# Kernel optimization log

Hardware: AMD Instinct MI355X
Metric: run time of the kernel (lower is better)

Reference implementation:

```python
import jax, jax.numpy as jnp
import numpy as np

LOAD_BALANCE_WEIGHT = 0.05


def setup_inputs() -> dict:
    key = jax.random.key(0)
    ks = jax.random.split(key, 8)
    B, H, C, E = 8192, 4096, 1000, 4
    s_h = 1.0 / np.sqrt(H)
    return {
        "x": jax.random.normal(ks[0], (B, H), dtype=jnp.float32),
        "Wr": jax.random.normal(ks[1], (H, E), dtype=jnp.float32) * s_h,
        "br": jnp.zeros((E,), dtype=jnp.float32),
        "W1": jax.random.normal(ks[2], (E, H, H), dtype=jnp.float32) * s_h,
        "b1": jnp.zeros((E, H), dtype=jnp.float32),
        "W2": jax.random.normal(ks[3], (E, H, C), dtype=jnp.float32) * s_h,
        "b2": jnp.zeros((E, C), dtype=jnp.float32),
    }


def reference(x, Wr, br, W1, b1, W2, b2):
    # Router: linear gate -> softmax probs (eval mode: no noise)
    E = Wr.shape[1]
    router_logits = x @ Wr + br                     # [B, E]
    routing_weights = jax.nn.softmax(router_logits, axis=-1)
    # Hard top-1 dispatch
    idx = jnp.argmax(routing_weights, axis=-1)      # [B]
    onehot = jax.nn.one_hot(idx, E, dtype=x.dtype)  # [B, E]
    # Switch-style load-balance loss: E * sum(fraction_e * mean_prob_e)
    frac = onehot.mean(axis=0)                      # [E]
    mean_p = routing_weights.mean(axis=0)           # [E]
    load_balance_loss = LOAD_BALANCE_WEIGHT * E * jnp.sum(frac * mean_p)
    # Dense all-expert compute, then hard-select per token (same math as
    # gather/scatter dispatch in the torch loop, fully vectorized)
    h = jax.nn.gelu(jnp.einsum('bh,ehk->ebk', x, W1) + b1[:, None, :])  # [E,B,H]
    expert_out = jnp.einsum('ebk,ekc->ebc', h, W2) + b2[:, None, :]     # [E,B,C]
    logits = jnp.einsum('be,ebc->bc', onehot, expert_out)               # [B,C]
    return logits, load_balance_loss, routing_weights
```

## Files before the change

### kernel.cpp

```cpp
#include <hip/hip_runtime.h>
#include <hip/hip_bf16.h>

#define NB 8192
#define NH 4096
#define NC 1000
#define NE 4
#define NCP 1024

typedef __attribute__((ext_vector_type(4))) float f32x4;
typedef __attribute__((ext_vector_type(8))) short s16x8;
typedef __attribute__((ext_vector_type(4))) unsigned int u32x4;

__device__ __forceinline__ unsigned cvtpk(float a, float b){
  unsigned r; asm("v_cvt_pk_bf16_f32 %0, %1, %2" : "=v"(r) : "v"(a), "v"(b)); return r;
}
__device__ __forceinline__ int swz_off(int r, int s){
  return (r << 6) + (((s ^ (r ^ (r >> 2))) & 3) << 4);
}
__device__ __forceinline__ int fswz(int r){ return (r ^ (r >> 2)) & 3; }

__device__ __forceinline__ void gload16(const void* g, void* l) {
  __builtin_amdgcn_global_load_lds(
      (const __attribute__((address_space(1))) unsigned int*)g,
      (__attribute__((address_space(3))) unsigned int*)l, 16, 0, 0);
}

__global__ __launch_bounds__(256) void router2_k(
    const float* __restrict__ x, const float* __restrict__ Wr,
    const float* __restrict__ br, float* __restrict__ out,
    int* __restrict__ idx, int* __restrict__ cnt_part, float* __restrict__ sum_part,
    __hip_bfloat16* __restrict__ xb)
{
  int b = blockIdx.x, t = threadIdx.x;
  const float* xr = x + (size_t)b * NH;
  int h0 = t << 4;
  f32x4 v[4];
  #pragma unroll
  for (int j = 0; j < 4; j++) v[j] = *(const f32x4*)(xr + h0 + (j << 2));
  u32x4 ob0 = { cvtpk(v[0][0],v[0][1]), cvtpk(v[0][2],v[0][3]),
                cvtpk(v[1][0],v[1][1]), cvtpk(v[1][2],v[1][3]) };
  u32x4 ob1 = { cvtpk(v[2][0],v[2][1]), cvtpk(v[2][2],v[2][3]),
                cvtpk(v[3][0],v[3][1]), cvtpk(v[3][2],v[3][3]) };
  *(u32x4*)(xb + (size_t)b * NH + h0) = ob0;
  *(u32x4*)(xb + (size_t)b * NH + h0 + 8) = ob1;

  double a0=0, a1=0, a2=0, a3=0;
  #pragma unroll
  for (int i = 0; i < 16; i++) {
    float xv = v[i >> 2][i & 3];
    f32x4 w = *(const f32x4*)(Wr + (size_t)(h0 + i) * 4);
    double xd = (double)xv;
    a0 += xd * (double)w[0]; a1 += xd * (double)w[1];
    a2 += xd * (double)w[2]; a3 += xd * (double)w[3];
  }
  for (int off = 32; off; off >>= 1) {
    a0 += __shfl_down(a0, off); a1 += __shfl_down(a1, off);
    a2 += __shfl_down(a2, off); a3 += __shfl_down(a3, off);
  }
  __shared__ double red[4][4];
  int wid = t >> 6;
  if ((t & 63) == 0) { red[wid][0]=a0; red[wid][1]=a1; red[wid][2]=a2; red[wid][3]=a3; }
  __syncthreads();
  if (t == 0) {
    double l[4];
    for (int e = 0; e < 4; e++)
      l[e] = red[0][e] + red[1][e] + red[2][e] + red[3][e] + (double)br[e];
    int am = 0; double mx = l[0];
    for (int e = 1; e < 4; e++) if (l[e] > mx) { mx = l[e]; am = e; }
    double p[4], s = 0;
    for (int e = 0; e < 4; e++) { p[e] = exp(l[e] - mx); s += p[e]; }
    float* rw = out + (size_t)NB * NC + 1 + (size_t)b * 4;
    int bin = (b & 63) * 4;
    for (int e = 0; e < 4; e++) {
      float pe = (float)(p[e] / s);
      rw[e] = pe;
      atomicAdd(&sum_part[bin + e], pe);
    }
    idx[b] = am;
    atomicAdd(&cnt_part[bin + am], 1);
  }
}

__global__ __launch_bounds__(256) void router_k(
    const float* __restrict__ x, const float* __restrict__ Wr,
    const float* __restrict__ br, float* __restrict__ out,
    int* __restrict__ idx, int* __restrict__ cnt_part, float* __restrict__ sum_part)
{
  int b = blockIdx.x, t = threadIdx.x;
  const float* xr = x + (size_t)b * NH;
  double a0=0, a1=0, a2=0, a3=0;
  for (int i = 0; i < 16; i++) {
    int h = t + (i << 8);
    float xv = xr[h];
    f32x4 w = *(const f32x4*)(Wr + (size_t)h * 4);
    double xd = (double)xv;
    a0 += xd * (double)w[0]; a1 += xd * (double)w[1];
    a2 += xd * (double)w[2]; a3 += xd * (double)w[3];
  }
  for (int off = 32; off; off >>= 1) {
    a0 += __shfl_down(a0, off); a1 += __shfl_down(a1, off);
    a2 += __shfl_down(a2, off); a3 += __shfl_down(a3, off);
  }
  __shared__ double red[4][4];
  int wid = t >> 6;
  if ((t & 63) == 0) { red[wid][0]=a0; red[wid][1]=a1; red[wid][2]=a2; red[wid][3]=a3; }
  __syncthreads();
  if (t == 0) {
    double l[4];
    for (int e = 0; e < 4; e++)
      l[e] = red[0][e] + red[1][e] + red[2][e] + red[3][e] + (double)br[e];
    int am = 0; double mx = l[0];
    for (int e = 1; e < 4; e++) if (l[e] > mx) { mx = l[e]; am = e; }
    double p[4], s = 0;
    for (int e = 0; e < 4; e++) { p[e] = exp(l[e] - mx); s += p[e]; }
    float* rw = out + (size_t)NB * NC + 1 + (size_t)b * 4;
    int bin = (b & 63) * 4;
    for (int e = 0; e < 4; e++) {
      float pe = (float)(p[e] / s);
      rw[e] = pe;
      atomicAdd(&sum_part[bin + e], pe);
    }
    idx[b] = am;
    atomicAdd(&cnt_part[bin + am], 1);
  }
}

__global__ void finalize_k(const int* __restrict__ cnt_part, const float* __restrict__ sum_part,
                           int* __restrict__ counts, int* __restrict__ offs, float* __restrict__ out)
{
  int t = threadIdx.x;
  __shared__ int cc[4]; __shared__ float ss[4];
  if (t < 4) {
    int c = 0; float s = 0;
    for (int i = 0; i < 64; i++) { c += cnt_part[i*4 + t]; s += sum_part[i*4 + t]; }
    cc[t] = c; ss[t] = s; counts[t] = c;
  }
  __syncthreads();
  if (t == 0) {
    int o = 0; float loss = 0.f;
    for (int e = 0; e < 4; e++) {
      offs[e] = o; o += cc[e];
      loss += ((float)cc[e] / (float)NB) * (ss[e] / (float)NB);
    }
    out[(size_t)NB * NC] = 0.05f * (float)NE * loss;
  }
}

__global__ __launch_bounds__(256) void scatter_k(
    const int* __restrict__ idx, const int* __restrict__ offs,
    int* __restrict__ cursors, int* __restrict__ perm)
{
  int b = blockIdx.x * 256 + threadIdx.x;
  int e = idx[b];
  int lane = threadIdx.x & 63;
  for (int e2 = 0; e2 < 4; e2++) {
    unsigned long long m = __ballot(e == e2);
    if (e == e2) {
      int nbelow = __popcll(m & ((1ULL << lane) - 1ULL));
      int base = 0;
      if (nbelow == 0) base = atomicAdd(&cursors[e2], (int)__popcll(m));
      int src = __ffsll((long long)m) - 1;
      base = __shfl(base, src);
      perm[offs[e2] + base + nbelow] = b;
    }
  }
}

__global__ __launch_bounds__(256) void transpose_k(
    const float* __restrict__ in, __hip_bfloat16* __restrict__ outp,
    int R, int C, int Cout)
{
  int e = blockIdx.z;
  int r0 = blockIdx.y << 5;
  int c0 = blockIdx.x << 10;
  const float* ine = in + (size_t)e * R * C;
  __hip_bfloat16* oute = outp + (size_t)e * Cout * R;
  int t = threadIdx.x;
  int c = c0 + (t << 2);
  unsigned o[4][16];
  if (c < C) {
    #pragma unroll
    for (int rp = 0; rp < 16; rp++) {
      f32x4 v0 = *(const f32x4*)(ine + (size_t)(r0 + 2*rp)     * C + c);
      f32x4 v1 = *(const f32x4*)(ine + (size_t)(r0 + 2*rp + 1) * C + c);
      #pragma unroll
      for (int j = 0; j < 4; j++) o[j][rp] = cvtpk(v0[j], v1[j]);
    }
  } else {
    #pragma unroll
    for (int j = 0; j < 4; j++)
      #pragma unroll
      for (int rp = 0; rp < 16; rp++) o[j][rp] = 0;
  }
  #pragma unroll
  for (int j = 0; j < 4; j++) {
    u32x4* dst = (u32x4*)(oute + (size_t)(c + j) * R + r0);
    dst[0] = (u32x4){ o[j][0],  o[j][1],  o[j][2],  o[j][3]  };
    dst[1] = (u32x4){ o[j][4],  o[j][5],  o[j][6],  o[j][7]  };
    dst[2] = (u32x4){ o[j][8],  o[j][9],  o[j][10], o[j][11] };
    dst[3] = (u32x4){ o[j][12], o[j][13], o[j][14], o[j][15] };
  }
}

__global__ __launch_bounds__(256) void gemm1n_k(
    const __hip_bfloat16* __restrict__ xb, const __hip_bfloat16* __restrict__ W1t,
    const float* __restrict__ b1, const int* __restrict__ perm,
    const int* __restrict__ counts, const int* __restrict__ offs,
    __hip_bfloat16* __restrict__ H1)
{
  int e = blockIdx.z;
  int cnt = counts[e];
  int m0 = blockIdx.y << 7;
  if (m0 >= cnt) return;
  int seg = offs[e];
  int n0 = blockIdx.x << 7;
  const __hip_bfloat16* W1te = W1t + (size_t)e * NH * NH;

  __shared__ __align__(16) char As[8192];
  __shared__ __align__(16) char Bs[8192];
  __shared__ int rowtok[128];

  int t = threadIdx.x;
  if (t < 128) {
    int rr = m0 + t; if (rr >= cnt) rr = cnt - 1;
    rowtok[t] = perm[seg + rr];
  }
  __syncthreads();

  int r0 = t >> 2, s0 = t & 3;
  int r1 = r0 + 64;
  const __hip_bfloat16* pA0 = xb + (size_t)rowtok[r0] * NH + ((s0 ^ fswz(r0)) << 3);
  const __hip_bfloat16* pA1 = xb + (size_t)rowtok[r1] * NH + ((s0 ^ fswz(r1)) << 3);
  const __hip_bfloat16* pB0 = W1te + (size_t)(n0 + r0) * NH + ((s0 ^ fswz(r0)) << 3);
  const __hip_bfloat16* pB1 = W1te + (size_t)(n0 + r1) * NH + ((s0 ^ fswz(r1)) << 3);
  int wid = t >> 6;
  char* ldsA0 = As + (wid << 10);
  char* ldsA1 = As + 4096 + (wid << 10);
  char* ldsB0 = Bs + (wid << 10);
  char* ldsB1 = Bs + 4096 + (wid << 10);

  f32x4 acc[4][4] = {};

  int lane = t & 63;
  int wm = (wid >> 1) << 6, wn = (wid & 1) << 6;
  int g = lane >> 4, cx = lane & 15;
  int aoff[4], boff[4];
  #pragma unroll
  for (int f = 0; f < 4; f++) {
    aoff[f] = swz_off(wm + (f << 4) + cx, g);
    boff[f] = swz_off(wn + (f << 4) + cx, g);
  }

  for (int kt = 0; kt < NH; kt += 32) {
    gload16(pA0 + kt, ldsA0);
    gload16(pA1 + kt, ldsA1);
    gload16(pB0 + kt, ldsB0);
    gload16(pB1 + kt, ldsB1);
    __syncthreads();
    s16x8 af[4], bfr[4];
    #pragma unroll
    for (int f = 0; f < 4; f++) {
      af[f]  = *(const s16x8*)(As + aoff[f]);
      bfr[f] = *(const s16x8*)(Bs + boff[f]);
    }
    #pragma unroll
    for (int mf = 0; mf < 4; mf++)
      #pragma unroll
      for (int nf = 0; nf < 4; nf++)
        acc[mf][nf] = __builtin_amdgcn_mfma_f32_16x16x32_bf16(af[mf], bfr[nf], acc[mf][nf], 0, 0, 0);
    __syncthreads();
  }

  const float* b1e = b1 + (size_t)e * NH;
  #pragma unroll
  for (int nf = 0; nf < 4; nf++) {
    int n = n0 + wn + (nf << 4) + cx;
    float bias = b1e[n];
    #pragma unroll
    for (int mf = 0; mf < 4; mf++) {
      #pragma unroll
      for (int i = 0; i < 4; i++) {
        int mseg = m0 + wm + (mf << 4) + (g << 2) + i;
        if (mseg < cnt) {
          float u = acc[mf][nf][i] + bias;
          float th = tanhf(0.79788456080286535588f * (u + 0.044715f * u * u * u));
          float hv = 0.5f * u * (1.0f + th);
          H1[(size_t)(seg + mseg) * NH + n] = __float2bfloat16(hv);
        }
      }
    }
  }
}

__global__ __launch_bounds__(256) void gemm2n_k(
    const __hip_bfloat16* __restrict__ H1, const __hip_bfloat16* __restrict__ W2t,
    const float* __restrict__ b2, const int* __restrict__ perm,
    const int* __restrict__ counts, const int* __restrict__ offs,
    float* __restrict__ out)
{
  int e = blockIdx.z;
  int cnt = counts[e];
  int m0 = blockIdx.y << 7;
  if (m0 >= cnt) return;
  int seg = offs[e];
  int n0 = blockIdx.x << 7;
  const __hip_bfloat16* W2te = W2t + (size_t)e * NCP * NH;

  __shared__ __align__(16) char As[8192];
  __shared__ __align__(16) char Bs[8192];
  __shared__ int rowtok[128];

  int t = threadIdx.x;
  if (t < 128) {
    int rr = m0 + t; if (rr >= cnt) rr = cnt - 1;
    rowtok[t] = perm[seg + rr];
  }
  __syncthreads();

  int r0 = t >> 2, s0 = t & 3;
  int r1 = r0 + 64;
  int rA0 = m0 + r0; if (rA0 >= cnt) rA0 = cnt - 1;
  int rA1 = m0 + r1; if (rA1 >= cnt) rA1 = cnt - 1;
  const __hip_bfloat16* pA0 = H1 + (size_t)(seg + rA0) * NH + ((s0 ^ fswz(r0)) << 3);
  const __hip_bfloat16* pA1 = H1 + (size_t)(seg + rA1) * NH + ((s0 ^ fswz(r1)) << 3);
  const __hip_bfloat16* pB0 = W2te + (size_t)(n0 + r0) * NH + ((s0 ^ fswz(r0)) << 3);
  const __hip_bfloat16* pB1 = W2te + (size_t)(n0 + r1) * NH + ((s0 ^ fswz(r1)) << 3);
  int wid = t >> 6;
  char* ldsA0 = As + (wid << 10);
  char* ldsA1 = As + 4096 + (wid << 10);
  char* ldsB0 = Bs + (wid << 10);
  char* ldsB1 = Bs + 4096 + (wid << 10);

  f32x4 acc[4][4] = {};

  int lane = t & 63;
  int wm = (wid >> 1) << 6, wn = (wid & 1) << 6;
  int g = lane >> 4, cx = lane & 15;
  int aoff[4], boff[4];
  #pragma unroll
  for (int f = 0; f < 4; f++) {
    aoff[f] = swz_off(wm + (f << 4) + cx, g);
    boff[f] = swz_off(wn + (f << 4) + cx, g);
  }

  for (int kt = 0; kt < NH; kt += 32) {
    gload16(pA0 + kt, ldsA0);
    gload16(pA1 + kt, ldsA1);
    gload16(pB0 + kt, ldsB0);
    gload16(pB1 + kt, ldsB1);
    __syncthreads();
    s16x8 af[4], bfr[4];
    #pragma unroll
    for (int f = 0; f < 4; f++) {
      af[f]  = *(const s16x8*)(As + aoff[f]);
      bfr[f] = *(const s16x8*)(Bs + boff[f]);
    }
    #pragma unroll
    for (int mf = 0; mf < 4; mf++)
      #pragma unroll
      for (int nf = 0; nf < 4; nf++)
        acc[mf][nf] = __builtin_amdgcn_mfma_f32_16x16x32_bf16(af[mf], bfr[nf], acc[mf][nf], 0, 0, 0);
    __syncthreads();
  }

  const float* b2e = b2 + (size_t)e * NC;
  #pragma unroll
  for (int nf = 0; nf < 4; nf++) {
    int n = n0 + wn + (nf << 4) + cx;
    if (n < NC) {
      float bias = b2e[n];
      #pragma unroll
      for (int mf = 0; mf < 4; mf++) {
        #pragma unroll
        for (int i = 0; i < 4; i++) {
          int mseg = m0 + wm + (mf << 4) + (g << 2) + i;
          if (mseg < cnt) {
            int tok = rowtok[wm + (mf << 4) + (g << 2) + i];
            out[(size_t)tok * NC + n] = acc[mf][nf][i] + bias;
          }
        }
      }
    }
  }
}

__global__ __launch_bounds__(256) void gemm1_k(
    const float* __restrict__ x, const float* __restrict__ W1,
    const float* __restrict__ b1, const int* __restrict__ perm,
    const int* __restrict__ counts, const int* __restrict__ offs,
    __hip_bfloat16* __restrict__ H1)
{
  int e = blockIdx.z;
  int cnt = counts[e];
  int m0 = blockIdx.y << 7;
  if (m0 >= cnt) return;
  int seg = offs[e];
  int n0 = blockIdx.x << 7;
  const float* W1e = W1 + (size_t)e * NH * NH;

  __shared__ __align__(16) char As[128*32*2];
  __shared__ __align__(16) char Bs[128*32*2];
  __shared__ int rowtok[128];

  int t = threadIdx.x;
  if (t < 128) {
    int rr = m0 + t; if (rr >= cnt) rr = cnt - 1;
    rowtok[t] = perm[seg + rr];
  }
  __syncthreads();

  int ar0 = t >> 2, as_ = t & 3;
  int ar1 = ar0 + 64;
  const float* asrc0 = x + (size_t)rowtok[ar0] * NH + (as_ << 3);
  const float* asrc1 = x + (size_t)rowtok[ar1] * NH + (as_ << 3);
  int aw0 = swz_off(ar0, as_), aw1 = swz_off(ar1, as_);
  int bnc = t & 31, bkp = t >> 5;
  const float* bsrc0 = W1e + (size_t)(bkp << 1) * NH + n0 + (bnc << 2);
  const float* bsrc1 = bsrc0 + (size_t)16 * NH;

  f32x4 acc[4][4] = {};

  int lane = t & 63, wid = t >> 6;
  int wm = (wid >> 1) << 6, wn = (wid & 1) << 6;
  int g = lane >> 4, cx = lane & 15;
  int aoff[4], boff[4];
  #pragma unroll
  for (int f = 0; f < 4; f++) {
    aoff[f] = swz_off(wm + (f << 4) + cx, g);
    boff[f] = swz_off(wn + (f << 4) + cx, g);
  }

  for (int kt = 0; kt < NH; kt += 32) {
    {
      f32x4 v0 = *(const f32x4*)(asrc0 + kt);
      f32x4 v1 = *(const f32x4*)(asrc0 + kt + 4);
      u32x4 w = { cvtpk(v0[0],v0[1]), cvtpk(v0[2],v0[3]), cvtpk(v1[0],v1[1]), cvtpk(v1[2],v1[3]) };
      *(u32x4*)(As + aw0) = w;
      f32x4 u0 = *(const f32x4*)(asrc1 + kt);
      f32x4 u1 = *(const f32x4*)(asrc1 + kt + 4);
      u32x4 w2 = { cvtpk(u0[0],u0[1]), cvtpk(u0[2],u0[3]), cvtpk(u1[0],u1[1]), cvtpk(u1[2],u1[3]) };
      *(u32x4*)(As + aw1) = w2;
    }
    {
      const float* p0 = bsrc0 + (size_t)kt * NH;
      f32x4 rr0 = *(const f32x4*)p0;
      f32x4 rr1 = *(const f32x4*)(p0 + NH);
      int kp = bkp, sl = kp >> 2, sub = (kp & 3) << 2;
      #pragma unroll
      for (int j = 0; j < 4; j++) {
        int n = (bnc << 2) + j;
        *(unsigned*)(Bs + (n << 6) + (((sl ^ (n ^ (n >> 2))) & 3) << 4) + sub) = cvtpk(rr0[j], rr1[j]);
      }
      const float* p1 = bsrc1 + (size_t)kt * NH;
      f32x4 q0 = *(const f32x4*)p1;
      f32x4 q1 = *(const f32x4*)(p1 + NH);
      kp = bkp + 8; sl = kp >> 2; sub = (kp & 3) << 2;
      #pragma unroll
      for (int j = 0; j < 4; j++) {
        int n = (bnc << 2) + j;
        *(unsigned*)(Bs + (n << 6) + (((sl ^ (n ^ (n >> 2))) & 3) << 4) + sub) = cvtpk(q0[j], q1[j]);
      }
    }
    __syncthreads();
    s16x8 af[4], bfr[4];
    #pragma unroll
    for (int f = 0; f < 4; f++) {
      af[f]  = *(const s16x8*)(As + aoff[f]);
      bfr[f] = *(const s16x8*)(Bs + boff[f]);
    }
    #pragma unroll
    for (int mf = 0; mf < 4; mf++)
      #pragma unroll
      for (int nf = 0; nf < 4; nf++)
        acc[mf][nf] = __builtin_amdgcn_mfma_f32_16x16x32_bf16(af[mf], bfr[nf], acc[mf][nf], 0, 0, 0);
    __syncthreads();
  }

  const float* b1e = b1 + (size_t)e * NH;
  #pragma unroll
  for (int nf = 0; nf < 4; nf++) {
    int n = n0 + wn + (nf << 4) + cx;
    float bias = b1e[n];
    #pragma unroll
    for (int mf = 0; mf < 4; mf++) {
      #pragma unroll
      for (int i = 0; i < 4; i++) {
        int mseg = m0 + wm + (mf << 4) + (g << 2) + i;
        if (mseg < cnt) {
          float u = acc[mf][nf][i] + bias;
          float th = tanhf(0.79788456080286535588f * (u + 0.044715f * u * u * u));
          float hv = 0.5f * u * (1.0f + th);
          H1[(size_t)(seg + mseg) * NH + n] = __float2bfloat16(hv);
        }
      }
    }
  }
}

__global__ __launch_bounds__(256) void gemm2_k(
    const __hip_bfloat16* __restrict__ H1, const float* __restrict__ W2,
    const float* __restrict__ b2, const int* __restrict__ perm,
    const int* __restrict__ counts, const int* __restrict__ offs,
    float* __restrict__ out)
{
  int e = blockIdx.z;
  int cnt = counts[e];
  int m0 = blockIdx.y << 7;
  if (m0 >= cnt) return;
  int seg = offs[e];
  int n0 = blockIdx.x << 7;
  const float* W2e = W2 + (size_t)e * NH * NC;

  __shared__ __align__(16) char As[128*32*2];
  __shared__ __align__(16) char Bs[128*32*2];
  __shared__ int rowtok[128];

  int t = threadIdx.x;
  if (t < 128) {
    int rr = m0 + t; if (rr >= cnt) rr = cnt - 1;
    rowtok[t] = perm[seg + rr];
  }
  __syncthreads();

  int ar0 = t >> 2, as_ = t & 3;
  int ar1 = ar0 + 64;
  int rA0 = m0 + ar0; if (rA0 >= cnt) rA0 = cnt - 1;
  int rA1 = m0 + ar1; if (rA1 >= cnt) rA1 = cnt - 1;
  const __hip_bfloat16* asrc0 = H1 + (size_t)(seg + rA0) * NH + (as_ << 3);
  const __hip_bfloat16* asrc1 = H1 + (size_t)(seg + rA1) * NH + (as_ << 3);
  int aw0 = swz_off(ar0, as_), aw1 = swz_off(ar1, as_);

  int bnc = t & 31, bkp = t >> 5;
  int col = n0 + (bnc << 2);
  bool bvalid = col < NC;
  const float* bsrc0 = W2e + (size_t)(bkp << 1) * NC + col;
  const float* bsrc1 = bsrc0 + (size_t)16 * NC;

  f32x4 acc[4][4] = {};

  int lane = t & 63, wid = t >> 6;
  int wm = (wid >> 1) << 6, wn = (wid & 1) << 6;
  int g = lane >> 4, cx = lane & 15;
  int aoff[4], boff[4];
  #pragma unroll
  for (int f = 0; f < 4; f++) {
    aoff[f] = swz_off(wm + (f << 4) + cx, g);
    boff[f] = swz_off(wn + (f << 4) + cx, g);
  }

  for (int kt = 0; kt < NH; kt += 32) {
    {
      *(u32x4*)(As + aw0) = *(const u32x4*)(asrc0 + kt);
      *(u32x4*)(As + aw1) = *(const u32x4*)(asrc1 + kt);
    }
    {
      f32x4 rr0 = {}, rr1 = {}, q0 = {}, q1 = {};
      if (bvalid) {
        const float* p0 = bsrc0 + (size_t)kt * NC;
        rr0 = *(const f32x4*)p0; rr1 = *(const f32x4*)(p0 + NC);
        const float* p1 = bsrc1 + (size_t)kt * NC;
        q0 = *(const f32x4*)p1; q1 = *(const f32x4*)(p1 + NC);
      }
      int kp = bkp, sl = kp >> 2, sub = (kp & 3) << 2;
      #pragma unroll
      for (int j = 0; j < 4; j++) {
        int n = (bnc << 2) + j;
        *(unsigned*)(Bs + (n << 6) + (((sl ^ (n ^ (n >> 2))) & 3) << 4) + sub) = cvtpk(rr0[j], rr1[j]);
      }
      kp = bkp + 8; sl = kp >> 2; sub = (kp & 3) << 2;
      #pragma unroll
      for (int j = 0; j < 4; j++) {
        int n = (bnc << 2) + j;
        *(unsigned*)(Bs + (n << 6) + (((sl ^ (n ^ (n >> 2))) & 3) << 4) + sub) = cvtpk(q0[j], q1[j]);
      }
    }
    __syncthreads();
    s16x8 af[4], bfr[4];
    #pragma unroll
    for (int f = 0; f < 4; f++) {
      af[f]  = *(const s16x8*)(As + aoff[f]);
      bfr[f] = *(const s16x8*)(Bs + boff[f]);
    }
    #pragma unroll
    for (int mf = 0; mf < 4; mf++)
      #pragma unroll
      for (int nf = 0; nf < 4; nf++)
        acc[mf][nf] = __builtin_amdgcn_mfma_f32_16x16x32_bf16(af[mf], bfr[nf], acc[mf][nf], 0, 0, 0);
    __syncthreads();
  }

  const float* b2e = b2 + (size_t)e * NC;
  #pragma unroll
  for (int nf = 0; nf < 4; nf++) {
    int n = n0 + wn + (nf << 4) + cx;
    if (n < NC) {
      float bias = b2e[n];
      #pragma unroll
      for (int mf = 0; mf < 4; mf++) {
        #pragma unroll
        for (int i = 0; i < 4; i++) {
          int mseg = m0 + wm + (mf << 4) + (g << 2) + i;
          if (mseg < cnt) {
            int tok = rowtok[wm + (mf << 4) + (g << 2) + i];
            out[(size_t)tok * NC + n] = acc[mf][nf][i] + bias;
          }
        }
      }
    }
  }
}

extern "C" void kernel_launch(void* const* d_in, const int* in_sizes, int n_in,
                              void* d_out, int out_size, void* d_ws, size_t ws_size,
                              hipStream_t stream) {
  const float* x  = (const float*)d_in[0];
  const float* Wr = (const float*)d_in[1];
  const float* br = (const float*)d_in[2];
  const float* W1 = (const float*)d_in[3];
  const float* b1 = (const float*)d_in[4];
  const float* W2 = (const float*)d_in[5];
  const float* b2 = (const float*)d_in[6];
  float* out = (float*)d_out;

  char* ws = (char*)d_ws;
  const size_t SZ_XB  = (size_t)NB * NH * 2;
  const size_t SZ_H1  = (size_t)NB * NH * 2;
  const size_t SZ_W1T = (size_t)NE * NH * NH * 2;
  const size_t SZ_W2T = (size_t)NE * NCP * NH * 2;
  const size_t need = SZ_XB + SZ_H1 + SZ_W1T + SZ_W2T + (size_t)NB*4*2 + 4096;

  if (ws_size >= need) {
    size_t o = 0;
    __hip_bfloat16* xb  = (__hip_bfloat16*)(ws + o); o += SZ_XB;
    __hip_bfloat16* H1  = (__hip_bfloat16*)(ws + o); o += SZ_H1;
    __hip_bfloat16* W1t = (__hip_bfloat16*)(ws + o); o += SZ_W1T;
    __hip_bfloat16* W2t = (__hip_bfloat16*)(ws + o); o += SZ_W2T;
    int* idx  = (int*)(ws + o); o += (size_t)NB * 4;
    int* perm = (int*)(ws + o); o += (size_t)NB * 4;
    char* small = ws + o;
    int*   cursors  = (int*)(small);
    int*   counts   = (int*)(small + 16);
    int*   offs     = (int*)(small + 32);
    int*   cnt_part = (int*)(small + 64);
    float* sum_part = (float*)(small + 64 + 1024);

    hipMemsetAsync(small, 0, 64 + 2048, stream);
    transpose_k<<<dim3(4, 128, 4), 256, 0, stream>>>(W1, W1t, NH, NH, NH);
    transpose_k<<<dim3(1, 128, 4), 256, 0, stream>>>(W2, W2t, NH, NC, NCP);
    router2_k<<<NB, 256, 0, stream>>>(x, Wr, br, out, idx, cnt_part, sum_part, xb);
    finalize_k<<<1, 64, 0, stream>>>(cnt_part, sum_part, counts, offs, out);
    scatter_k<<<NB / 256, 256, 0, stream>>>(idx, offs, cursors, perm);
    gemm1n_k<<<dim3(32, 64, 4), 256, 0, stream>>>(xb, W1t, b1, perm, counts, offs, H1);
    gemm2n_k<<<dim3(8, 64, 4), 256, 0, stream>>>(H1, W2t, b2, perm, counts, offs, out);
  } else {
    __hip_bfloat16* H1 = (__hip_bfloat16*)ws;
    size_t o = (size_t)NB * NH * 2;
    int* idx  = (int*)(ws + o); o += (size_t)NB * 4;
    int* perm = (int*)(ws + o); o += (size_t)NB * 4;
    char* small = ws + o;
    int*   cursors  = (int*)(small);
    int*   counts   = (int*)(small + 16);
    int*   offs     = (int*)(small + 32);
    int*   cnt_part = (int*)(small + 64);
    float* sum_part = (float*)(small + 64 + 1024);

    hipMemsetAsync(small, 0, 64 + 2048, stream);
    router_k<<<NB, 256, 0, stream>>>(x, Wr, br, out, idx, cnt_part, sum_part);
    finalize_k<<<1, 64, 0, stream>>>(cnt_part, sum_part, counts, offs, out);
    scatter_k<<<NB / 256, 256, 0, stream>>>(idx, offs, cursors, perm);
    gemm1_k<<<dim3(32, 64, 4), 256, 0, stream>>>(x, W1, b1, perm, counts, offs, H1);
    gemm2_k<<<dim3(8, 64, 4), 256, 0, stream>>>(H1, W2, b2, perm, counts, offs, out);
  }
}
```

Measured before the change: 788.9 us.

## Replace grouped expert GEMMs with 256x256 double-buffered phased MFMA kernel

Replaces the two separate 128x128, K=32, single-buffered expert GEMM kernels with one templated kernel. The new kernel uses 256x256 tiles, 512 threads, K=64 stages and a double-buffered 128KB LDS ring. The main loop is split into phases that interleave global-to-LDS loads for later stages with MFMA work, using explicit vmcnt waits, barriers and s_setprio, so memory latency hides behind compute and each loaded tile is reused more. In exchange, the large LDS footprint limits each CU to one block, and the hand-scheduled waitcnt pipeline is fragile.

Result: slower. 982.9 us (+24.6%).

```diff
diff --git a/kernel.cpp b/kernel.cpp
--- a/kernel.cpp
+++ b/kernel.cpp
@@ -17,7 +17,6 @@
 __device__ __forceinline__ int swz_off(int r, int s){
   return (r << 6) + (((s ^ (r ^ (r >> 2))) & 3) << 4);
 }
-__device__ __forceinline__ int fswz(int r){ return (r ^ (r >> 2)) & 3; }
 
 __device__ __forceinline__ void gload16(const void* g, void* l) {
   __builtin_amdgcn_global_load_lds(
@@ -202,181 +201,164 @@
   }
 }
 
-__global__ __launch_bounds__(256) void gemm1n_k(
-    const __hip_bfloat16* __restrict__ xb, const __hip_bfloat16* __restrict__ W1t,
-    const float* __restrict__ b1, const int* __restrict__ perm,
+
+#define DSR(off) (*(const s16x8*)(lds + (off)))
+#define FENCE() asm volatile("" ::: "memory")
+#define VMW(N) asm volatile("s_waitcnt vmcnt(" #N ")" ::: "memory")
+
+#define STAGE_A(TT,H) do { \
+  gload16(((H) ? pA1c0 : pA0c0) + (size_t)(TT)*64, lds + (((TT)&1)*32768 + (H)*16384 + wld)); \
+  gload16(((H) ? pA1c1 : pA0c1) + (size_t)(TT)*64, lds + (((TT)&1)*32768 + (H)*16384 + wld + 1024)); \
+} while(0)
+#define STAGE_B(TT,H) do { \
+  gload16(((H) ? pB1c0 : pB0c0) + (size_t)(TT)*64, lds + (65536 + ((TT)&1)*32768 + (H)*16384 + wld)); \
+  gload16(((H) ? pB1c1 : pB0c1) + (size_t)(TT)*64, lds + (65536 + ((TT)&1)*32768 + (H)*16384 + wld + 1024)); \
+} while(0)
+#define NOSTAGE do{}while(0)
+
+#define PHASE(BB, MH, NHQ, STAGE_STMT, WAIT_STMT) do { \
+  s16x8 a_[4][2], b_[2][2]; \
+  _Pragma("unroll") \
+  for (int mf = 0; mf < 4; mf++) { \
+    a_[mf][0] = DSR((BB)*32768 + (MH)*16384 + arow_ + mf*2048 + swz0); \
+    a_[mf][1] = DSR((BB)*32768 + (MH)*16384 + arow_ + mf*2048 + swz1); \
+  } \
+  _Pragma("unroll") \
+  for (int nf = 0; nf < 2; nf++) { \
+    b_[nf][0] = DSR(65536 + (BB)*32768 + (NHQ)*16384 + brow_ + nf*2048 + swz0); \
+    b_[nf][1] = DSR(65536 + (BB)*32768 + (NHQ)*16384 + brow_ + nf*2048 + swz1); \
+  } \
+  STAGE_STMT; \
+  WAIT_STMT; \
+  __builtin_amdgcn_s_barrier(); \
+  __builtin_amdgcn_sched_barrier(0); \
+  __builtin_amdgcn_s_setprio(1); \
+  _Pragma("unroll") \
+  for (int mf = 0; mf < 4; mf++) \
+    _Pragma("unroll") \
+    for (int nf = 0; nf < 2; nf++) { \
+      acc[(MH)*2+(NHQ)][mf][nf] = __builtin_amdgcn_mfma_f32_16x16x32_bf16(a_[mf][0], b_[nf][0], acc[(MH)*2+(NHQ)][mf][nf], 0, 0, 0); \
+      acc[(MH)*2+(NHQ)][mf][nf] = __builtin_amdgcn_mfma_f32_16x16x32_bf16(a_[mf][1], b_[nf][1], acc[(MH)*2+(NHQ)][mf][nf], 0, 0, 0); \
+    } \
+  __builtin_amdgcn_s_setprio(0); \
+  __builtin_amdgcn_s_barrier(); \
+  FENCE(); \
+} while(0)
+
+template<int MODE>
+__global__ __launch_bounds__(512, 2) void gemm8p_k(
+    const __hip_bfloat16* __restrict__ Ax, const __hip_bfloat16* __restrict__ Bw,
+    const float* __restrict__ bias, const int* __restrict__ perm,
     const int* __restrict__ counts, const int* __restrict__ offs,
-    __hip_bfloat16* __restrict__ H1)
+    __hip_bfloat16* __restrict__ H1out, float* __restrict__ out)
 {
   int e = blockIdx.z;
   int cnt = counts[e];
-  int m0 = blockIdx.y << 7;
+  if (cnt == 0) return;
+  int m0 = blockIdx.y << 8;
   if (m0 >= cnt) return;
   int seg = offs[e];
-  int n0 = blockIdx.x << 7;
-  const __hip_bfloat16* W1te = W1t + (size_t)e * NH * NH;
-
-  __shared__ __align__(16) char As[8192];
-  __shared__ __align__(16) char Bs[8192];
-  __shared__ int rowtok[128];
+  int n0 = blockIdx.x << 8;
+  const __hip_bfloat16* Be = Bw + (size_t)e * (size_t)(MODE == 0 ? NH : NCP) * NH;
+
+  __shared__ __align__(16) char lds[131072];
+  __shared__ int rowtok[256];
 
   int t = threadIdx.x;
-  if (t < 128) {
+  if (t < 256) {
     int rr = m0 + t; if (rr >= cnt) rr = cnt - 1;
     rowtok[t] = perm[seg + rr];
   }
   __syncthreads();
 
-  int r0 = t >> 2, s0 = t & 3;
-  int r1 = r0 + 64;
-  const __hip_bfloat16* pA0 = xb + (size_t)rowtok[r0] * NH + ((s0 ^ fswz(r0)) << 3);
-  const __hip_bfloat16* pA1 = xb + (size_t)rowtok[r1] * NH + ((s0 ^ fswz(r1)) << 3);
-  const __hip_bfloat16* pB0 = W1te + (size_t)(n0 + r0) * NH + ((s0 ^ fswz(r0)) << 3);
-  const __hip_bfloat16* pB1 = W1te + (size_t)(n0 + r1) * NH + ((s0 ^ fswz(r1)) << 3);
-  int wid = t >> 6;
-  char* ldsA0 = As + (wid << 10);
-  char* ldsA1 = As + 4096 + (wid << 10);
-  char* ldsB0 = Bs + (wid << 10);
-  char* ldsB1 = Bs + 4096 + (wid << 10);
-
-  f32x4 acc[4][4] = {};
-
-  int lane = t & 63;
-  int wm = (wid >> 1) << 6, wn = (wid & 1) << 6;
-  int g = lane >> 4, cx = lane & 15;
-  int aoff[4], boff[4];
-  #pragma unroll
-  for (int f = 0; f < 4; f++) {
-    aoff[f] = swz_off(wm + (f << 4) + cx, g);
-    boff[f] = swz_off(wn + (f << 4) + cx, g);
-  }
-
-  for (int kt = 0; kt < NH; kt += 32) {
-    gload16(pA0 + kt, ldsA0);
-    gload16(pA1 + kt, ldsA1);
-    gload16(pB0 + kt, ldsB0);
-    gload16(pB1 + kt, ldsB1);
-    __syncthreads();
-    s16x8 af[4], bfr[4];
-    #pragma unroll
-    for (int f = 0; f < 4; f++) {
-      af[f]  = *(const s16x8*)(As + aoff[f]);
-      bfr[f] = *(const s16x8*)(Bs + boff[f]);
-    }
-    #pragma unroll
-    for (int mf = 0; mf < 4; mf++)
-      #pragma unroll
-      for (int nf = 0; nf < 4; nf++)
-        acc[mf][nf] = __builtin_amdgcn_mfma_f32_16x16x32_bf16(af[mf], bfr[nf], acc[mf][nf], 0, 0, 0);
-    __syncthreads();
-  }
-
-  const float* b1e = b1 + (size_t)e * NH;
-  #pragma unroll
-  for (int nf = 0; nf < 4; nf++) {
-    int n = n0 + wn + (nf << 4) + cx;
-    float bias = b1e[n];
-    #pragma unroll
-    for (int mf = 0; mf < 4; mf++) {
-      #pragma unroll
-      for (int i = 0; i < 4; i++) {
-        int mseg = m0 + wm + (mf << 4) + (g << 2) + i;
-        if (mseg < cnt) {
-          float u = acc[mf][nf][i] + bias;
-          float th = tanhf(0.79788456080286535588f * (u + 0.044715f * u * u * u));
-          float hv = 0.5f * u * (1.0f + th);
-          H1[(size_t)(seg + mseg) * NH + n] = __float2bfloat16(hv);
-        }
-      }
-    }
-  }
-}
-
-__global__ __launch_bounds__(256) void gemm2n_k(
-    const __hip_bfloat16* __restrict__ H1, const __hip_bfloat16* __restrict__ W2t,
-    const float* __restrict__ b2, const int* __restrict__ perm,
-    const int* __restrict__ counts, const int* __restrict__ offs,
-    float* __restrict__ out)
-{
-  int e = blockIdx.z;
-  int cnt = counts[e];
-  int m0 = blockIdx.y << 7;
-  if (m0 >= cnt) return;
-  int seg = offs[e];
-  int n0 = blockIdx.x << 7;
-  const __hip_bfloat16* W2te = W2t + (size_t)e * NCP * NH;
-
-  __shared__ __align__(16) char As[8192];
-  __shared__ __align__(16) char Bs[8192];
-  __shared__ int rowtok[128];
-
-  int t = threadIdx.x;
-  if (t < 128) {
-    int rr = m0 + t; if (rr >= cnt) rr = cnt - 1;
-    rowtok[t] = perm[seg + rr];
-  }
-  __syncthreads();
-
-  int r0 = t >> 2, s0 = t & 3;
-  int r1 = r0 + 64;
-  int rA0 = m0 + r0; if (rA0 >= cnt) rA0 = cnt - 1;
-  int rA1 = m0 + r1; if (rA1 >= cnt) rA1 = cnt - 1;
-  const __hip_bfloat16* pA0 = H1 + (size_t)(seg + rA0) * NH + ((s0 ^ fswz(r0)) << 3);
-  const __hip_bfloat16* pA1 = H1 + (size_t)(seg + rA1) * NH + ((s0 ^ fswz(r1)) << 3);
-  const __hip_bfloat16* pB0 = W2te + (size_t)(n0 + r0) * NH + ((s0 ^ fswz(r0)) << 3);
-  const __hip_bfloat16* pB1 = W2te + (size_t)(n0 + r1) * NH + ((s0 ^ fswz(r1)) << 3);
-  int wid = t >> 6;
-  char* ldsA0 = As + (wid << 10);
-  char* ldsA1 = As + 4096 + (wid << 10);
-  char* ldsB0 = Bs + (wid << 10);
-  char* ldsB1 = Bs + 4096 + (wid << 10);
-
-  f32x4 acc[4][4] = {};
-
-  int lane = t & 63;
-  int wm = (wid >> 1) << 6, wn = (wid & 1) << 6;
-  int g = lane >> 4, cx = lane & 15;
-  int aoff[4], boff[4];
-  #pragma unroll
-  for (int f = 0; f < 4; f++) {
-    aoff[f] = swz_off(wm + (f << 4) + cx, g);
-    boff[f] = swz_off(wn + (f << 4) + cx, g);
-  }
-
-  for (int kt = 0; kt < NH; kt += 32) {
-    gload16(pA0 + kt, ldsA0);
-    gload16(pA1 + kt, ldsA1);
-    gload16(pB0 + kt, ldsB0);
-    gload16(pB1 + kt, ldsB1);
-    __syncthreads();
-    s16x8 af[4], bfr[4];
-    #pragma unroll
-    for (int f = 0; f < 4; f++) {
-      af[f]  = *(const s16x8*)(As + aoff[f]);
-      bfr[f] = *(const s16x8*)(Bs + boff[f]);
-    }
-    #pragma unroll
-    for (int mf = 0; mf < 4; mf++)
-      #pragma unroll
-      for (int nf = 0; nf < 4; nf++)
-        acc[mf][nf] = __builtin_amdgcn_mfma_f32_16x16x32_bf16(af[mf], bfr[nf], acc[mf][nf], 0, 0, 0);
-    __syncthreads();
-  }
-
-  const float* b2e = b2 + (size_t)e * NC;
-  #pragma unroll
-  for (int nf = 0; nf < 4; nf++) {
-    int n = n0 + wn + (nf << 4) + cx;
-    if (n < NC) {
-      float bias = b2e[n];
+  int lane = t & 63, w = t >> 6;
+  int wr = w >> 2, wc = w & 3;
+  int cx = lane & 15, g = lane >> 4;
+  int l8 = lane >> 3, l7 = lane & 7;
+
+  int srcoff = (l7 ^ l8) << 3;
+  int ra = w * 16 + l8;
+  const __hip_bfloat16 *pA0c0, *pA0c1, *pA1c0, *pA1c1;
+  if constexpr (MODE == 0) {
+    pA0c0 = Ax + (size_t)rowtok[ra      ] * NH + srcoff;
+    pA0c1 = Ax + (size_t)rowtok[ra +   8] * NH + srcoff;
+    pA1c0 = Ax + (size_t)rowtok[ra + 128] * NH + srcoff;
+    pA1c1 = Ax + (size_t)rowtok[ra + 136] * NH + srcoff;
+  } else {
+    int r0c0 = m0 + ra;       if (r0c0 >= cnt) r0c0 = cnt - 1;
+    int r0c1 = m0 + ra + 8;   if (r0c1 >= cnt) r0c1 = cnt - 1;
+    int r1c0 = m0 + ra + 128; if (r1c0 >= cnt) r1c0 = cnt - 1;
+    int r1c1 = m0 + ra + 136; if (r1c1 >= cnt) r1c1 = cnt - 1;
+    pA0c0 = Ax + (size_t)(seg + r0c0) * NH + srcoff;
+    pA0c1 = Ax + (size_t)(seg + r0c1) * NH + srcoff;
+    pA1c0 = Ax + (size_t)(seg + r1c0) * NH + srcoff;
+    pA1c1 = Ax + (size_t)(seg + r1c1) * NH + srcoff;
+  }
+  const __hip_bfloat16 *pB0c0 = Be + (size_t)(n0 + ra      ) * NH + srcoff;
+  const __hip_bfloat16 *pB0c1 = Be + (size_t)(n0 + ra +   8) * NH + srcoff;
+  const __hip_bfloat16 *pB1c0 = Be + (size_t)(n0 + ra + 128) * NH + srcoff;
+  const __hip_bfloat16 *pB1c1 = Be + (size_t)(n0 + ra + 136) * NH + srcoff;
+  int wld = w * 2048;
+
+  int swz0 = ((0 * 4 + g) ^ (cx & 7)) << 4;
+  int swz1 = ((1 * 4 + g) ^ (cx & 7)) << 4;
+  int arow_ = (wr * 64 + cx) * 128;
+  int brow_ = (wc * 32 + cx) * 128;
+
+  f32x4 acc[4][4][2] = {};
+
+  const int NT = NH / 64;
+
+  STAGE_A(0,0); STAGE_B(0,0); STAGE_B(0,1); STAGE_A(0,1); STAGE_A(1,0); STAGE_B(1,0);
+  VMW(8);
+  __builtin_amdgcn_s_barrier();
+  __builtin_amdgcn_sched_barrier(0);
+
+  for (int tt = 0; tt < NT - 2; tt += 2) {
+    PHASE(0, 0, 0, STAGE_B(tt+1,1), VMW(8));
+    PHASE(0, 0, 1, STAGE_A(tt+1,1), VMW(8));
+    PHASE(0, 1, 0, STAGE_A(tt+2,0), VMW(8));
+    PHASE(0, 1, 1, STAGE_B(tt+2,0), VMW(8));
+    PHASE(1, 0, 0, STAGE_B(tt+2,1), VMW(8));
+    PHASE(1, 0, 1, STAGE_A(tt+2,1), VMW(8));
+    PHASE(1, 1, 0, STAGE_A(tt+3,0), VMW(8));
+    PHASE(1, 1, 1, STAGE_B(tt+3,0), VMW(8));
+  }
+  PHASE(0, 0, 0, STAGE_B(NT-1,1), VMW(8));
+  PHASE(0, 0, 1, STAGE_A(NT-1,1), VMW(8));
+  PHASE(0, 1, 0, NOSTAGE, VMW(6));
+  PHASE(0, 1, 1, NOSTAGE, VMW(4));
+  PHASE(1, 0, 0, NOSTAGE, VMW(2));
+  PHASE(1, 0, 1, NOSTAGE, VMW(0));
+  PHASE(1, 1, 0, NOSTAGE, FENCE());
+  PHASE(1, 1, 1, NOSTAGE, FENCE());
+
+  #pragma unroll
+  for (int mh = 0; mh < 2; mh++)
+  #pragma unroll
+  for (int nh = 0; nh < 2; nh++)
+  #pragma unroll
+  for (int nf = 0; nf < 2; nf++) {
+    int n = n0 + nh * 128 + wc * 32 + nf * 16 + cx;
+    if (MODE == 0 || n < NC) {
+      float bv = bias[(size_t)e * (MODE == 0 ? NH : NC) + n];
       #pragma unroll
       for (int mf = 0; mf < 4; mf++) {
+        f32x4 vacc = acc[mh*2+nh][mf][nf];
         #pragma unroll
         for (int i = 0; i < 4; i++) {
-          int mseg = m0 + wm + (mf << 4) + (g << 2) + i;
+          int mrow = mh * 128 + wr * 64 + mf * 16 + g * 4 + i;
+          int mseg = m0 + mrow;
           if (mseg < cnt) {
-            int tok = rowtok[wm + (mf << 4) + (g << 2) + i];
-            out[(size_t)tok * NC + n] = acc[mf][nf][i] + bias;
+            float u = vacc[i] + bv;
+            if constexpr (MODE == 0) {
+              float th = tanhf(0.79788456080286535588f * (u + 0.044715f * u * u * u));
+              float hv = 0.5f * u * (1.0f + th);
+              H1out[(size_t)(seg + mseg) * NH + n] = __float2bfloat16(hv);
+            } else {
+              int tok = rowtok[mrow];
+              out[(size_t)tok * NC + n] = u;
+            }
           }
         }
       }
@@ -434,8 +416,8 @@
     {
       f32x4 v0 = *(const f32x4*)(asrc0 + kt);
       f32x4 v1 = *(const f32x4*)(asrc0 + kt + 4);
-      u32x4 w = { cvtpk(v0[0],v0[1]), cvtpk(v0[2],v0[3]), cvtpk(v1[0],v1[1]), cvtpk(v1[2],v1[3]) };
-      *(u32x4*)(As + aw0) = w;
+      u32x4 wv = { cvtpk(v0[0],v0[1]), cvtpk(v0[2],v0[3]), cvtpk(v1[0],v1[1]), cvtpk(v1[2],v1[3]) };
+      *(u32x4*)(As + aw0) = wv;
       f32x4 u0 = *(const f32x4*)(asrc1 + kt);
       f32x4 u1 = *(const f32x4*)(asrc1 + kt + 4);
       u32x4 w2 = { cvtpk(u0[0],u0[1]), cvtpk(u0[2],u0[3]), cvtpk(u1[0],u1[1]), cvtpk(u1[2],u1[3]) };
@@ -480,14 +462,14 @@
   #pragma unroll
   for (int nf = 0; nf < 4; nf++) {
     int n = n0 + wn + (nf << 4) + cx;
-    float bias = b1e[n];
+    float bv = b1e[n];
     #pragma unroll
     for (int mf = 0; mf < 4; mf++) {
       #pragma unroll
       for (int i = 0; i < 4; i++) {
         int mseg = m0 + wm + (mf << 4) + (g << 2) + i;
         if (mseg < cnt) {
-          float u = acc[mf][nf][i] + bias;
+          float u = acc[mf][nf][i] + bv;
           float th = tanhf(0.79788456080286535588f * (u + 0.044715f * u * u * u));
           float hv = 0.5f * u * (1.0f + th);
           H1[(size_t)(seg + mseg) * NH + n] = __float2bfloat16(hv);
@@ -594,7 +576,7 @@
   for (int nf = 0; nf < 4; nf++) {
     int n = n0 + wn + (nf << 4) + cx;
     if (n < NC) {
-      float bias = b2e[n];
+      float bv = b2e[n];
       #pragma unroll
       for (int mf = 0; mf < 4; mf++) {
         #pragma unroll
@@ -602,7 +584,7 @@
           int mseg = m0 + wm + (mf << 4) + (g << 2) + i;
           if (mseg < cnt) {
             int tok = rowtok[wm + (mf << 4) + (g << 2) + i];
-            out[(size_t)tok * NC + n] = acc[mf][nf][i] + bias;
+            out[(size_t)tok * NC + n] = acc[mf][nf][i] + bv;
           }
         }
       }
@@ -650,8 +632,8 @@
     router2_k<<<NB, 256, 0, stream>>>(x, Wr, br, out, idx, cnt_part, sum_part, xb);
     finalize_k<<<1, 64, 0, stream>>>(cnt_part, sum_part, counts, offs, out);
     scatter_k<<<NB / 256, 256, 0, stream>>>(idx, offs, cursors, perm);
-    gemm1n_k<<<dim3(32, 64, 4), 256, 0, stream>>>(xb, W1t, b1, perm, counts, offs, H1);
-    gemm2n_k<<<dim3(8, 64, 4), 256, 0, stream>>>(H1, W2t, b2, perm, counts, offs, out);
+    gemm8p_k<0><<<dim3(16, 32, 4), 512, 0, stream>>>(xb, W1t, b1, perm, counts, offs, H1, nullptr);
+    gemm8p_k<1><<<dim3(4, 32, 4), 512, 0, stream>>>(H1, W2t, b2, perm, counts, offs, nullptr, out);
   } else {
     __hip_bfloat16* H1 = (__hip_bfloat16*)ws;
     size_t o = (size_t)NB * NH * 2;
```
